# Kernel tuning notes

Hardware: AMD Instinct MI355X
Metric: run time of the kernel (lower is better)

## Reference

```python
import jax, jax.numpy as jnp
import numpy as np

LN_EPS = 1e-5


def _ln(h, g, b):
    mu = h.mean(-1, keepdims=True)
    var = ((h - mu) ** 2).mean(-1, keepdims=True)
    return (h - mu) / jnp.sqrt(var + LN_EPS) * g + b


def setup_inputs() -> dict:
    key = jax.random.key(0)
    ks = jax.random.split(key, 12)
    B, T, Cin, C, D, M = 16, 1024, 512, 1024, 256, 1024
    s = 0.02
    inp = {
        "x": jax.random.normal(ks[0], (B, T, Cin), jnp.float32),
        "masks": jnp.ones((B, T), jnp.float32),
        "W1": jax.random.normal(ks[1], (Cin, C), jnp.float32) * s,
        "g1": jnp.ones((C,), jnp.float32), "b1": jnp.zeros((C,), jnp.float32),
        "W2": jax.random.normal(ks[2], (C, C), jnp.float32) * s,
        "g2": jnp.ones((C,), jnp.float32), "b2": jnp.zeros((C,), jnp.float32),
        "W3": jax.random.normal(ks[3], (C, C), jnp.float32) * s,
        "g3": jnp.ones((C,), jnp.float32), "b3": jnp.zeros((C,), jnp.float32),
        "W4": jax.random.normal(ks[4], (C, C), jnp.float32) * s,
        "g4": jnp.ones((C,), jnp.float32), "b4": jnp.zeros((C,), jnp.float32),
        "W5": jax.random.normal(ks[5], (C, D), jnp.float32) * s,
        "b5": jnp.zeros((D,), jnp.float32),
        # Dirichlet(alpha=100) rows, as in the torch init: rows live on the simplex
        "embedding": jax.random.dirichlet(ks[6], jnp.full((D,), 100.0, jnp.float32), (M,)).astype(jnp.float32),
    }
    return inp


def reference(x, masks, W1, g1, b1, W2, g2, b2, W3, g3, b3, W4, g4, b4, W5, b5, embedding):
    h = jax.nn.relu(_ln(x @ W1, g1, b1))
    h = jax.nn.relu(_ln(h @ W2, g2, b2))
    h = jax.nn.relu(_ln(h @ W3, g3, b3))
    h = jax.nn.relu(_ln(h @ W4, g4, b4))
    z = h @ W5 + b5                              # [B, T, D]
    p = jax.nn.log_softmax(z, axis=-1)           # log-prob features

    B, T, D = p.shape
    p_flat = jax.lax.stop_gradient(p.reshape(-1, D))   # x.detach() in torch
    ep = jnp.exp(p_flat)                               # [N, D]
    # KL(exp(p) || e_m) summed over D, for all codes m:
    #   sum_d exp(p)*(p - log(e_m)) = rowsum(exp(p)*p) - exp(p) @ log(E)^T
    div = (ep * p_flat).sum(-1, keepdims=True) - ep @ jnp.log(embedding).T  # [N, M]
    idx = jnp.argmin(div, axis=-1)                     # [N]
    quant = jax.lax.stop_gradient(embedding[idx].reshape(B, T, D))

    # commitment loss: masked KL(exp(p) || quant.detach())
    kl = (jnp.exp(p) * (p - jnp.log(quant))).sum(-1)   # [B, T]
    loss = 0.25 * (kl * masks).mean(0).sum()

    # straight-through estimator
    q = p + jax.lax.stop_gradient(quant - p)
    return z, q, loss
```

## Files before the change

### kernel.cpp

```cpp
#include <hip/hip_runtime.h>
#include <hip/hip_bf16.h>
#include <stdint.h>

typedef __attribute__((ext_vector_type(4))) float f32x4;
typedef __attribute__((ext_vector_type(8))) __bf16 bf16x8;
typedef __attribute__((ext_vector_type(4))) __bf16 bf16x4;

#define LN_EPS 1e-5f

__device__ __forceinline__ void gload_lds16(const void* g, void* l) {
  __builtin_amdgcn_global_load_lds(
      (__attribute__((address_space(1))) void*)(uintptr_t)g,
      (__attribute__((address_space(3))) void*)(uint32_t)(uintptr_t)l,
      16, 0, 0);
}

__device__ __forceinline__ f32x4 mfma16(bf16x8 a, bf16x8 b, f32x4 c) {
  return __builtin_amdgcn_mfma_f32_16x16x32_bf16(a, b, c, 0, 0, 0);
}

__global__ __launch_bounds__(256) void k_cvt_bf16(const float* __restrict__ x,
                                                  __bf16* __restrict__ o) {
  int i = (blockIdx.x * 256 + threadIdx.x) * 8;
  f32x4 a = *(const f32x4*)(x + i);
  f32x4 b = *(const f32x4*)(x + i + 4);
  bf16x8 v;
#pragma unroll
  for (int j = 0; j < 4; ++j) { v[j] = (__bf16)a[j]; v[j + 4] = (__bf16)b[j]; }
  *(bf16x8*)(o + i) = v;
}

__global__ void k_transpose(const float* __restrict__ W, __bf16* __restrict__ Wt,
                            int K, int N) {
  __shared__ float t[32][33];
  int nt = blockIdx.x * 32, kt = blockIdx.y * 32;
  int tx = threadIdx.x, ty = threadIdx.y;
  t[ty][tx] = W[(size_t)(kt + ty) * N + nt + tx];
  __syncthreads();
  Wt[(size_t)(nt + ty) * K + kt + tx] = (__bf16)t[tx][ty];
}

__global__ void k_transpose3(const float* __restrict__ Wa, const float* __restrict__ Wb,
                             const float* __restrict__ Wc, __bf16* __restrict__ Ta,
                             __bf16* __restrict__ Tb, __bf16* __restrict__ Tc) {
  __shared__ float t[32][33];
  const float* W = blockIdx.z == 0 ? Wa : (blockIdx.z == 1 ? Wb : Wc);
  __bf16* T = blockIdx.z == 0 ? Ta : (blockIdx.z == 1 ? Tb : Tc);
  int nt = blockIdx.x * 32, kt = blockIdx.y * 32;
  int tx = threadIdx.x, ty = threadIdx.y;
  t[ty][tx] = W[(size_t)(kt + ty) * 1024 + nt + tx];
  __syncthreads();
  T[(size_t)(nt + ty) * 1024 + kt + tx] = (__bf16)t[tx][ty];
}

__global__ __launch_bounds__(256) void k_logE(const float* __restrict__ e,
                                              __bf16* __restrict__ o) {
  int i = blockIdx.x * 256 + threadIdx.x;
  o[i] = (__bf16)logf(e[i] * 256.0f);
}

__global__ __launch_bounds__(512, 2) void k_gemm256(
    const __bf16* __restrict__ A, const __bf16* __restrict__ Bt,
    __bf16* __restrict__ O, int N, int K) {
  __shared__ char lds[131072];
  const int tid = threadIdx.x;
  const int lane = tid & 63;
  const int wid = tid >> 6;
  const int wm = wid >> 2;
  const int wn = wid & 3;
  const int bm0 = blockIdx.x * 256;
  const int bn0 = blockIdx.y * 256;
  const int NT = K >> 6;

  const int slin = tid * 16;
  const int lrow = slin >> 7;
  const int scol = (slin & 127) ^ ((lrow & 7) << 4);
  const char* Ab = (const char*)A;
  const char* Bb = (const char*)Bt;
  const uint32_t rs = (uint32_t)K * 2;

  const int klo = (lane >> 4) * 16;
  const int sw = (lane & 7) << 4;
  const uint32_t kx0 = (uint32_t)(klo ^ sw);
  const uint32_t kx1 = (uint32_t)((64 + klo) ^ sw);
  const uint32_t abase = (uint32_t)(wm * 128 + (lane & 15)) * 128;
  const uint32_t bbase = (uint32_t)(wn * 64 + (lane & 15)) * 128;

  f32x4 acc[8][4];
#pragma unroll
  for (int i = 0; i < 8; ++i)
#pragma unroll
    for (int j = 0; j < 4; ++j) acc[i][j] = 0.0f;

#define LDSA(buf) (lds + (buf)*32768)
#define LDSB(buf) (lds + 65536 + (buf)*32768)
#define STAGE_A(t, h)                                                              \
  {                                                                                \
    const char* src = Ab + (size_t)(bm0 + (h)*128 + lrow) * rs + ((t) << 7) + scol;\
    char* dst = LDSA((t)&1) + (h)*16384 + slin;                                    \
    gload_lds16(src, dst);                                                         \
    gload_lds16(src + (size_t)64 * rs, dst + 8192);                                \
  }
#define STAGE_B(t, h)                                                              \
  {                                                                                \
    const char* src = Bb + (size_t)(bn0 + (h)*128 + lrow) * rs + ((t) << 7) + scol;\
    char* dst = LDSB((t)&1) + (h)*16384 + slin;                                    \
    gload_lds16(src, dst);                                                         \
    gload_lds16(src + (size_t)64 * rs, dst + 8192);                                \
  }

  STAGE_A(0, 0); STAGE_A(0, 1); STAGE_B(0, 0); STAGE_B(0, 1);
  STAGE_B(1, 0); STAGE_B(1, 1);
  asm volatile("s_waitcnt vmcnt(4)" ::: "memory");
  __builtin_amdgcn_s_barrier();
  asm volatile("" ::: "memory");

  for (int t = 0; t < NT; ++t) {
    const char* Acur = LDSA(t & 1);
    const char* Bcur = LDSB(t & 1);
    bf16x8 bF[4][2];
#pragma unroll
    for (int p = 0; p < 4; ++p) {
      const uint32_t ar = abase + (uint32_t)(2 * p) * 2048;
      bf16x8 a00 = *(const bf16x8*)(Acur + ar + kx0);
      bf16x8 a01 = *(const bf16x8*)(Acur + ar + kx1);
      bf16x8 a10 = *(const bf16x8*)(Acur + ar + 2048 + kx0);
      bf16x8 a11 = *(const bf16x8*)(Acur + ar + 2048 + kx1);
      if (p == 0) {
#pragma unroll
        for (int ni = 0; ni < 4; ++ni) {
          bF[ni][0] = *(const bf16x8*)(Bcur + bbase + ni * 2048 + kx0);
          bF[ni][1] = *(const bf16x8*)(Bcur + bbase + ni * 2048 + kx1);
        }
      }
      if (p == 0 && t + 1 < NT) STAGE_A(t + 1, 0);
      if (p == 1) {
        if (t + 1 < NT) STAGE_A(t + 1, 1);
        if (t + 2 < NT) STAGE_B(t + 2, 0);
      }
      if (p == 2 && t + 2 < NT) STAGE_B(t + 2, 1);

      asm volatile("" ::: "memory");
      __builtin_amdgcn_s_barrier();
      asm volatile("" ::: "memory");
      __builtin_amdgcn_s_setprio(1);
#pragma unroll
      for (int ni = 0; ni < 4; ++ni) {
        acc[2 * p][ni] = mfma16(a00, bF[ni][0], acc[2 * p][ni]);
        acc[2 * p][ni] = mfma16(a01, bF[ni][1], acc[2 * p][ni]);
        acc[2 * p + 1][ni] = mfma16(a10, bF[ni][0], acc[2 * p + 1][ni]);
        acc[2 * p + 1][ni] = mfma16(a11, bF[ni][1], acc[2 * p + 1][ni]);
      }
      __builtin_amdgcn_s_setprio(0);
      if (p == 3) asm volatile("s_waitcnt vmcnt(4)" ::: "memory");
      asm volatile("" ::: "memory");
      __builtin_amdgcn_s_barrier();
      asm volatile("" ::: "memory");
    }
  }
#undef STAGE_A
#undef STAGE_B
#undef LDSA
#undef LDSB

  const int r0 = (lane >> 4) * 4;
  const int cc = lane & 15;
#pragma unroll
  for (int mi = 0; mi < 8; ++mi) {
#pragma unroll
    for (int ni = 0; ni < 4; ++ni) {
      int r = bm0 + wm * 128 + mi * 16 + r0;
      int c = bn0 + wn * 64 + ni * 16 + cc;
#pragma unroll
      for (int j = 0; j < 4; ++j)
        O[(size_t)(r + j) * N + c] = (__bf16)acc[mi][ni][j];
    }
  }
}

template <int EPI>
__global__ __launch_bounds__(256) void k_gemm(
    const __bf16* __restrict__ A, const __bf16* __restrict__ Bt,
    void* __restrict__ outp, const float* __restrict__ bias,
    float* __restrict__ part_val, int* __restrict__ part_idx,
    int N, int K) {
  __shared__ char lds[32768];
  char* ldsA = lds;
  char* ldsB = lds + 16384;
  const int tid = threadIdx.x;
  const int lane = tid & 63;
  const int wid = tid >> 6;
  const int wm = wid >> 1, wn = wid & 1;
  const int bm0 = blockIdx.x * 128;
  const int bn0 = blockIdx.y * 128;

  const int slin = tid * 16;
  const int srow = slin >> 7;
  const int scol = (slin & 127) ^ ((srow & 7) << 4);

  const char* Ab = (const char*)A;
  const char* Bb = (const char*)Bt;
  const uint32_t rs = (uint32_t)K * 2;

  uint32_t ra[2][4], rb[2][4];
  {
    const int sw = (lane & 7) << 4;
    const int gk = lane & 48;
#pragma unroll
    for (int kk = 0; kk < 2; ++kk) {
#pragma unroll
      for (int i = 0; i < 4; ++i) {
        uint32_t kb = (uint32_t)((kk * 64 + gk) ^ sw);
        ra[kk][i] = (uint32_t)(wm * 64 + i * 16 + (lane & 15)) * 128 + kb;
        rb[kk][i] = (uint32_t)(wn * 64 + i * 16 + (lane & 15)) * 128 + kb;
      }
    }
  }

  f32x4 acc[4][4];
#pragma unroll
  for (int i = 0; i < 4; ++i)
#pragma unroll
    for (int j = 0; j < 4; ++j) acc[i][j] = 0.0f;

  for (int k0 = 0; k0 < K; k0 += 64) {
    __syncthreads();
    const uint32_t kbyte = (uint32_t)k0 * 2 + (uint32_t)scol;
#pragma unroll
    for (int i = 0; i < 4; ++i) {
      int row = i * 32 + srow;
      gload_lds16(Ab + (size_t)(bm0 + row) * rs + kbyte, ldsA + i * 4096 + slin);
    }
#pragma unroll
    for (int i = 0; i < 4; ++i) {
      int row = i * 32 + srow;
      gload_lds16(Bb + (size_t)(bn0 + row) * rs + kbyte, ldsB + i * 4096 + slin);
    }
    __syncthreads();
#pragma unroll
    for (int kk = 0; kk < 2; ++kk) {
      bf16x8 af[4], bfv[4];
#pragma unroll
      for (int i = 0; i < 4; ++i) af[i] = *(const bf16x8*)(ldsA + ra[kk][i]);
#pragma unroll
      for (int i = 0; i < 4; ++i) bfv[i] = *(const bf16x8*)(ldsB + rb[kk][i]);
#pragma unroll
      for (int mi = 0; mi < 4; ++mi)
#pragma unroll
        for (int ni = 0; ni < 4; ++ni)
          acc[mi][ni] = mfma16(af[mi], bfv[ni], acc[mi][ni]);
    }
  }

  const int r0 = (lane >> 4) * 4;
  const int cc = lane & 15;

  if constexpr (EPI == 1) {
    float* O = (float*)outp;
#pragma unroll
    for (int mi = 0; mi < 4; ++mi) {
#pragma unroll
      for (int ni = 0; ni < 4; ++ni) {
        int r = bm0 + wm * 64 + mi * 16 + r0;
        int c = bn0 + wn * 64 + ni * 16 + cc;
        float bv = bias[c];
#pragma unroll
        for (int j = 0; j < 4; ++j)
          O[(size_t)(r + j) * N + c] = acc[mi][ni][j] + bv;
      }
    }
  } else {
    const int nch = N >> 6;
#pragma unroll
    for (int mi = 0; mi < 4; ++mi) {
#pragma unroll
      for (int j = 0; j < 4; ++j) {
        float v = acc[mi][0][j];
        int c = cc;
#pragma unroll
        for (int ni = 1; ni < 4; ++ni) {
          float v2 = acc[mi][ni][j];
          int c2 = ni * 16 + cc;
          if (v2 > v) { v = v2; c = c2; }
        }
#pragma unroll
        for (int d = 1; d < 16; d <<= 1) {
          float ov = __shfl_xor(v, d);
          int oc = __shfl_xor(c, d);
          if (ov > v || (ov == v && oc < c)) { v = ov; c = oc; }
        }
        if (cc == 0) {
          int r = bm0 + wm * 64 + mi * 16 + r0 + j;
          int chunk = (bn0 >> 6) + wn;
          part_val[r * nch + chunk] = v;
          part_idx[r * nch + chunk] = bn0 + wn * 64 + c;
        }
      }
    }
  }
}

__global__ __launch_bounds__(256) void k_ln_relu(__bf16* __restrict__ h,
                                                 const float* __restrict__ g,
                                                 const float* __restrict__ b) {
  int lane = threadIdx.x & 63;
  int row = blockIdx.x * 4 + (threadIdx.x >> 6);
  __bf16* rp = h + (size_t)row * 1024;
  bf16x8 v0 = *(const bf16x8*)(rp + lane * 8);
  bf16x8 v1 = *(const bf16x8*)(rp + 512 + lane * 8);
  float f0[8], f1[8];
  float s = 0.f, sq = 0.f;
#pragma unroll
  for (int j = 0; j < 8; ++j) {
    f0[j] = (float)v0[j]; f1[j] = (float)v1[j];
    s += f0[j] + f1[j];
    sq += f0[j] * f0[j] + f1[j] * f1[j];
  }
#pragma unroll
  for (int d = 1; d < 64; d <<= 1) { s += __shfl_xor(s, d); sq += __shfl_xor(sq, d); }
  float mu = s * (1.0f / 1024.0f);
  float var = sq * (1.0f / 1024.0f) - mu * mu;
  float rstd = rsqrtf(var + LN_EPS);
  const f32x4* gv = (const f32x4*)g;
  const f32x4* bv = (const f32x4*)b;
  f32x4 ga0 = gv[lane * 2], ga1 = gv[lane * 2 + 1];
  f32x4 gb0 = gv[128 + lane * 2], gb1 = gv[128 + lane * 2 + 1];
  f32x4 ba0 = bv[lane * 2], ba1 = bv[lane * 2 + 1];
  f32x4 bb0 = bv[128 + lane * 2], bb1 = bv[128 + lane * 2 + 1];
  bf16x8 o0, o1;
#pragma unroll
  for (int j = 0; j < 4; ++j) {
    float t0 = (f0[j] - mu) * rstd * ga0[j] + ba0[j];
    float t1 = (f0[j + 4] - mu) * rstd * ga1[j] + ba1[j];
    float t2 = (f1[j] - mu) * rstd * gb0[j] + bb0[j];
    float t3 = (f1[j + 4] - mu) * rstd * gb1[j] + bb1[j];
    o0[j] = (__bf16)fmaxf(t0, 0.f);
    o0[j + 4] = (__bf16)fmaxf(t1, 0.f);
    o1[j] = (__bf16)fmaxf(t2, 0.f);
    o1[j + 4] = (__bf16)fmaxf(t3, 0.f);
  }
  *(bf16x8*)(rp + lane * 8) = o0;
  *(bf16x8*)(rp + 512 + lane * 8) = o1;
}

__global__ __launch_bounds__(256) void k_softmax(const float* __restrict__ z,
                                                 float* __restrict__ p,
                                                 __bf16* __restrict__ ep) {
  int lane = threadIdx.x & 63;
  int row = blockIdx.x * 4 + (threadIdx.x >> 6);
  f32x4 v = ((const f32x4*)(z + (size_t)row * 256))[lane];
  float m = fmaxf(fmaxf(v[0], v[1]), fmaxf(v[2], v[3]));
#pragma unroll
  for (int d = 1; d < 64; d <<= 1) m = fmaxf(m, __shfl_xor(m, d));
  f32x4 e;
  float s = 0.f;
#pragma unroll
  for (int j = 0; j < 4; ++j) { e[j] = expf(v[j] - m); s += e[j]; }
#pragma unroll
  for (int d = 1; d < 64; d <<= 1) s += __shfl_xor(s, d);
  float ls = logf(s);
  float inv = 1.0f / s;
  f32x4 pv;
  bf16x4 ev;
#pragma unroll
  for (int j = 0; j < 4; ++j) { pv[j] = v[j] - m - ls; ev[j] = (__bf16)(e[j] * inv); }
  ((f32x4*)(p + (size_t)row * 256))[lane] = pv;
  ((bf16x4*)(ep + (size_t)row * 256))[lane] = ev;
}

__global__ __launch_bounds__(256) void k_final(
    const float* __restrict__ part_val, const int* __restrict__ part_idx,
    const float* __restrict__ p, const float* __restrict__ emb,
    const float* __restrict__ masks, float* __restrict__ q,
    float* __restrict__ blockloss) {
  __shared__ float ls[4];
  int lane = threadIdx.x & 63;
  int w = threadIdx.x >> 6;
  int row = blockIdx.x * 4 + w;
  float v = -3.4e38f;
  int c = 0x7fffffff;
  if (lane < 16) { v = part_val[row * 16 + lane]; c = part_idx[row * 16 + lane]; }
#pragma unroll
  for (int d = 1; d < 16; d <<= 1) {
    float ov = __shfl_xor(v, d);
    int oc = __shfl_xor(c, d);
    if (ov > v || (ov == v && oc < c)) { v = ov; c = oc; }
  }
  int code = __shfl(c, 0);
  f32x4 ev = ((const f32x4*)(emb + (size_t)code * 256))[lane];
  ((f32x4*)(q + (size_t)row * 256))[lane] = ev;
  f32x4 pv = ((const f32x4*)(p + (size_t)row * 256))[lane];
  float kl = 0.f;
#pragma unroll
  for (int j = 0; j < 4; ++j) kl += expf(pv[j]) * (pv[j] - logf(ev[j]));
#pragma unroll
  for (int d = 1; d < 64; d <<= 1) kl += __shfl_xor(kl, d);
  if (lane == 0) ls[w] = kl * masks[row];
  __syncthreads();
  if (threadIdx.x == 0) blockloss[blockIdx.x] = ls[0] + ls[1] + ls[2] + ls[3];
}

__global__ __launch_bounds__(256) void k_loss_reduce(const float* __restrict__ bl,
                                                     float* __restrict__ out) {
  __shared__ float s[256];
  float a = 0.f;
#pragma unroll
  for (int i = 0; i < 16; ++i) a += bl[threadIdx.x + i * 256];
  s[threadIdx.x] = a;
  __syncthreads();
  for (int st = 128; st > 0; st >>= 1) {
    if (threadIdx.x < st) s[threadIdx.x] += s[threadIdx.x + st];
    __syncthreads();
  }
  if (threadIdx.x == 0) out[0] = s[0] * (0.25f / 16.0f);
}

extern "C" void kernel_launch(void* const* d_in, const int* in_sizes, int n_in,
                              void* d_out, int out_size, void* d_ws, size_t ws_size,
                              hipStream_t stream) {
  const float* x = (const float*)d_in[0];
  const float* masks = (const float*)d_in[1];
  const float* W1 = (const float*)d_in[2];
  const float* g1 = (const float*)d_in[3];
  const float* b1 = (const float*)d_in[4];
  const float* W2 = (const float*)d_in[5];
  const float* g2 = (const float*)d_in[6];
  const float* b2 = (const float*)d_in[7];
  const float* W3 = (const float*)d_in[8];
  const float* g3 = (const float*)d_in[9];
  const float* b3 = (const float*)d_in[10];
  const float* W4 = (const float*)d_in[11];
  const float* g4 = (const float*)d_in[12];
  const float* b4 = (const float*)d_in[13];
  const float* W5 = (const float*)d_in[14];
  const float* b5 = (const float*)d_in[15];
  const float* emb = (const float*)d_in[16];

  const int M = 16384;
  char* ws = (char*)d_ws;
  __bf16* bufA = (__bf16*)(ws);
  __bf16* bufB = (__bf16*)(ws + (32ull << 20));
  __bf16* W1t = (__bf16*)(ws + (64ull << 20));
  __bf16* W2t = (__bf16*)(ws + (65ull << 20));
  __bf16* W3t = (__bf16*)(ws + (67ull << 20));
  __bf16* W4t = (__bf16*)(ws + (69ull << 20));
  __bf16* W5t = (__bf16*)(ws + (71ull << 20));
  __bf16* logE = (__bf16*)(ws + (72ull << 20));
  float* part_val = (float*)(ws + (73ull << 20));
  int* part_idx = (int*)(ws + (74ull << 20));
  float* blockloss = (float*)(ws + (75ull << 20));
  float* p = (float*)(ws);
  __bf16* ep = (__bf16*)(ws + (16ull << 20));

  float* z = (float*)d_out;
  float* q = z + (size_t)M * 256;
  float* lossp = z + 2ull * M * 256;

  dim3 tb32(32, 32);
  k_cvt_bf16<<<4096, 256, 0, stream>>>(x, bufB);
  k_transpose<<<dim3(32, 16), tb32, 0, stream>>>(W1, W1t, 512, 1024);
  k_transpose3<<<dim3(32, 32, 3), tb32, 0, stream>>>(W2, W3, W4, W2t, W3t, W4t);
  k_transpose<<<dim3(8, 32), tb32, 0, stream>>>(W5, W5t, 1024, 256);
  k_logE<<<1024, 256, 0, stream>>>(emb, logE);

  k_gemm256<<<dim3(64, 4), 512, 0, stream>>>(bufB, W1t, bufA, 1024, 512);
  k_ln_relu<<<4096, 256, 0, stream>>>(bufA, g1, b1);
  k_gemm256<<<dim3(64, 4), 512, 0, stream>>>(bufA, W2t, bufB, 1024, 1024);
  k_ln_relu<<<4096, 256, 0, stream>>>(bufB, g2, b2);
  k_gemm256<<<dim3(64, 4), 512, 0, stream>>>(bufB, W3t, bufA, 1024, 1024);
  k_ln_relu<<<4096, 256, 0, stream>>>(bufA, g3, b3);
  k_gemm256<<<dim3(64, 4), 512, 0, stream>>>(bufA, W4t, bufB, 1024, 1024);
  k_ln_relu<<<4096, 256, 0, stream>>>(bufB, g4, b4);
  k_gemm<1><<<dim3(128, 2), 256, 0, stream>>>(bufB, W5t, z, b5, nullptr, nullptr, 256, 1024);
  k_softmax<<<4096, 256, 0, stream>>>(z, p, ep);
  k_gemm<2><<<dim3(128, 8), 256, 0, stream>>>(ep, logE, nullptr, nullptr, part_val, part_idx, 1024, 256);
  k_final<<<4096, 256, 0, stream>>>(part_val, part_idx, p, emb, masks, q, blockloss);
  k_loss_reduce<<<1, 256, 0, stream>>>(blockloss, lossp);
}
```

Before: 273.4 us.

## Fuse final projection GEMM with log-softmax and swizzle GEMM block order

The final Linear(C,D) GEMM now computes the full 256-wide output row per block and runs log-softmax in its epilogue. It writes z, bf16 probabilities and a per-row log-sum-exp, so the separate softmax kernel and the float p buffer are gone, and k_final rebuilds p from z minus the log-sum-exp. The 256x256 GEMMs also use a 1D grid with a swizzled block-to-tile mapping so that concurrently running blocks share A/B tiles in cache. The fused kernel uses 64-row tiles and loads all of W5 per k-step, which could lower MFMA efficiency for that GEMM.

Measured after the change: 281.4 us. 2.9% more time.

```diff
diff --git a/kernel.cpp b/kernel.cpp
--- a/kernel.cpp
+++ b/kernel.cpp
@@ -68,8 +68,9 @@
   const int wid = tid >> 6;
   const int wm = wid >> 2;
   const int wn = wid & 3;
-  const int bm0 = blockIdx.x * 256;
-  const int bn0 = blockIdx.y * 256;
+  const int swz = ((blockIdx.x & 7) << 5) | (blockIdx.x >> 3);
+  const int bm0 = (swz & 63) * 256;
+  const int bn0 = (swz >> 6) * 256;
   const int NT = K >> 6;
 
   const int slin = tid * 16;
@@ -174,128 +175,6 @@
 #pragma unroll
       for (int j = 0; j < 4; ++j)
         O[(size_t)(r + j) * N + c] = (__bf16)acc[mi][ni][j];
-    }
-  }
-}
-
-template <int EPI>
-__global__ __launch_bounds__(256) void k_gemm(
-    const __bf16* __restrict__ A, const __bf16* __restrict__ Bt,
-    void* __restrict__ outp, const float* __restrict__ bias,
-    float* __restrict__ part_val, int* __restrict__ part_idx,
-    int N, int K) {
-  __shared__ char lds[32768];
-  char* ldsA = lds;
-  char* ldsB = lds + 16384;
-  const int tid = threadIdx.x;
-  const int lane = tid & 63;
-  const int wid = tid >> 6;
-  const int wm = wid >> 1, wn = wid & 1;
-  const int bm0 = blockIdx.x * 128;
-  const int bn0 = blockIdx.y * 128;
-
-  const int slin = tid * 16;
-  const int srow = slin >> 7;
-  const int scol = (slin & 127) ^ ((srow & 7) << 4);
-
-  const char* Ab = (const char*)A;
-  const char* Bb = (const char*)Bt;
-  const uint32_t rs = (uint32_t)K * 2;
-
-  uint32_t ra[2][4], rb[2][4];
-  {
-    const int sw = (lane & 7) << 4;
-    const int gk = lane & 48;
-#pragma unroll
-    for (int kk = 0; kk < 2; ++kk) {
-#pragma unroll
-      for (int i = 0; i < 4; ++i) {
-        uint32_t kb = (uint32_t)((kk * 64 + gk) ^ sw);
-        ra[kk][i] = (uint32_t)(wm * 64 + i * 16 + (lane & 15)) * 128 + kb;
-        rb[kk][i] = (uint32_t)(wn * 64 + i * 16 + (lane & 15)) * 128 + kb;
-      }
-    }
-  }
-
-  f32x4 acc[4][4];
-#pragma unroll
-  for (int i = 0; i < 4; ++i)
-#pragma unroll
-    for (int j = 0; j < 4; ++j) acc[i][j] = 0.0f;
-
-  for (int k0 = 0; k0 < K; k0 += 64) {
-    __syncthreads();
-    const uint32_t kbyte = (uint32_t)k0 * 2 + (uint32_t)scol;
-#pragma unroll
-    for (int i = 0; i < 4; ++i) {
-      int row = i * 32 + srow;
-      gload_lds16(Ab + (size_t)(bm0 + row) * rs + kbyte, ldsA + i * 4096 + slin);
-    }
-#pragma unroll
-    for (int i = 0; i < 4; ++i) {
-      int row = i * 32 + srow;
-      gload_lds16(Bb + (size_t)(bn0 + row) * rs + kbyte, ldsB + i * 4096 + slin);
-    }
-    __syncthreads();
-#pragma unroll
-    for (int kk = 0; kk < 2; ++kk) {
-      bf16x8 af[4], bfv[4];
-#pragma unroll
-      for (int i = 0; i < 4; ++i) af[i] = *(const bf16x8*)(ldsA + ra[kk][i]);
-#pragma unroll
-      for (int i = 0; i < 4; ++i) bfv[i] = *(const bf16x8*)(ldsB + rb[kk][i]);
-#pragma unroll
-      for (int mi = 0; mi < 4; ++mi)
-#pragma unroll
-        for (int ni = 0; ni < 4; ++ni)
-          acc[mi][ni] = mfma16(af[mi], bfv[ni], acc[mi][ni]);
-    }
-  }
-
-  const int r0 = (lane >> 4) * 4;
-  const int cc = lane & 15;
-
-  if constexpr (EPI == 1) {
-    float* O = (float*)outp;
-#pragma unroll
-    for (int mi = 0; mi < 4; ++mi) {
-#pragma unroll
-      for (int ni = 0; ni < 4; ++ni) {
-        int r = bm0 + wm * 64 + mi * 16 + r0;
-        int c = bn0 + wn * 64 + ni * 16 + cc;
-        float bv = bias[c];
-#pragma unroll
-        for (int j = 0; j < 4; ++j)
-          O[(size_t)(r + j) * N + c] = acc[mi][ni][j] + bv;
-      }
-    }
-  } else {
-    const int nch = N >> 6;
-#pragma unroll
-    for (int mi = 0; mi < 4; ++mi) {
-#pragma unroll
-      for (int j = 0; j < 4; ++j) {
-        float v = acc[mi][0][j];
-        int c = cc;
-#pragma unroll
-        for (int ni = 1; ni < 4; ++ni) {
-          float v2 = acc[mi][ni][j];
-          int c2 = ni * 16 + cc;
-          if (v2 > v) { v = v2; c = c2; }
-        }
-#pragma unroll
-        for (int d = 1; d < 16; d <<= 1) {
-          float ov = __shfl_xor(v, d);
-          int oc = __shfl_xor(c, d);
-          if (ov > v || (ov == v && oc < c)) { v = ov; c = oc; }
-        }
-        if (cc == 0) {
-          int r = bm0 + wm * 64 + mi * 16 + r0 + j;
-          int chunk = (bn0 >> 6) + wn;
-          part_val[r * nch + chunk] = v;
-          part_idx[r * nch + chunk] = bn0 + wn * 64 + c;
-        }
-      }
     }
   }
 }
@@ -343,36 +222,257 @@
   *(bf16x8*)(rp + 512 + lane * 8) = o1;
 }
 
-__global__ __launch_bounds__(256) void k_softmax(const float* __restrict__ z,
-                                                 float* __restrict__ p,
-                                                 __bf16* __restrict__ ep) {
-  int lane = threadIdx.x & 63;
-  int row = blockIdx.x * 4 + (threadIdx.x >> 6);
-  f32x4 v = ((const f32x4*)(z + (size_t)row * 256))[lane];
-  float m = fmaxf(fmaxf(v[0], v[1]), fmaxf(v[2], v[3]));
-#pragma unroll
-  for (int d = 1; d < 64; d <<= 1) m = fmaxf(m, __shfl_xor(m, d));
-  f32x4 e;
-  float s = 0.f;
-#pragma unroll
-  for (int j = 0; j < 4; ++j) { e[j] = expf(v[j] - m); s += e[j]; }
-#pragma unroll
-  for (int d = 1; d < 64; d <<= 1) s += __shfl_xor(s, d);
-  float ls = logf(s);
-  float inv = 1.0f / s;
-  f32x4 pv;
-  bf16x4 ev;
-#pragma unroll
-  for (int j = 0; j < 4; ++j) { pv[j] = v[j] - m - ls; ev[j] = (__bf16)(e[j] * inv); }
-  ((f32x4*)(p + (size_t)row * 256))[lane] = pv;
-  ((bf16x4*)(ep + (size_t)row * 256))[lane] = ev;
+__global__ __launch_bounds__(256) void k_gemm_sm(
+    const __bf16* __restrict__ A, const __bf16* __restrict__ Bt,
+    const float* __restrict__ bias, float* __restrict__ z,
+    __bf16* __restrict__ ep, float* __restrict__ sm) {
+  const int K = 1024;
+  __shared__ char lds[40960];
+  char* ldsA = lds;
+  char* ldsB = lds + 8192;
+  const int tid = threadIdx.x;
+  const int lane = tid & 63;
+  const int wn = tid >> 6;
+  const int bm0 = blockIdx.x * 64;
+  const char* Ab = (const char*)A;
+  const char* Bb = (const char*)Bt;
+  const uint32_t rs = (uint32_t)K * 2;
+
+  const int cc = lane & 15;
+  uint32_t ra[2][4], rb[2][4];
+  {
+    const int sww = (lane & 7) << 4;
+    const int gk = lane & 48;
+#pragma unroll
+    for (int kk = 0; kk < 2; ++kk) {
+#pragma unroll
+      for (int i = 0; i < 4; ++i) {
+        uint32_t kb = (uint32_t)((kk * 64 + gk) ^ sww);
+        ra[kk][i] = (uint32_t)(i * 16 + cc) * 128 + kb;
+        rb[kk][i] = (uint32_t)(wn * 64 + i * 16 + cc) * 128 + kb;
+      }
+    }
+  }
+
+  f32x4 acc[4][4];
+#pragma unroll
+  for (int i = 0; i < 4; ++i)
+#pragma unroll
+    for (int j = 0; j < 4; ++j) acc[i][j] = 0.0f;
+
+  for (int k0 = 0; k0 < K; k0 += 64) {
+    __syncthreads();
+#pragma unroll
+    for (int i = 0; i < 2; ++i) {
+      int lin = i * 4096 + tid * 16;
+      int row = lin >> 7;
+      int col = (lin & 127) ^ ((row & 7) << 4);
+      gload_lds16(Ab + (size_t)(bm0 + row) * rs + k0 * 2 + col, ldsA + lin);
+    }
+#pragma unroll
+    for (int i = 0; i < 8; ++i) {
+      int lin = i * 4096 + tid * 16;
+      int row = lin >> 7;
+      int col = (lin & 127) ^ ((row & 7) << 4);
+      gload_lds16(Bb + (size_t)row * rs + k0 * 2 + col, ldsB + lin);
+    }
+    __syncthreads();
+#pragma unroll
+    for (int kk = 0; kk < 2; ++kk) {
+      bf16x8 af[4], bfv[4];
+#pragma unroll
+      for (int i = 0; i < 4; ++i) af[i] = *(const bf16x8*)(ldsA + ra[kk][i]);
+#pragma unroll
+      for (int i = 0; i < 4; ++i) bfv[i] = *(const bf16x8*)(ldsB + rb[kk][i]);
+#pragma unroll
+      for (int mi = 0; mi < 4; ++mi)
+#pragma unroll
+        for (int ni = 0; ni < 4; ++ni)
+          acc[mi][ni] = mfma16(af[mi], bfv[ni], acc[mi][ni]);
+    }
+  }
+
+  __syncthreads();
+  float* stm = (float*)lds;
+  float* sts = (float*)(lds + 1024);
+  float* rowm = (float*)(lds + 2048);
+  float* rows_ = (float*)(lds + 2304);
+
+  const int r0 = (lane >> 4) * 4;
+  float bvv[4];
+#pragma unroll
+  for (int ni = 0; ni < 4; ++ni) bvv[ni] = bias[wn * 64 + ni * 16 + cc];
+
+  float zv[4][4];
+#pragma unroll
+  for (int mi = 0; mi < 4; ++mi) {
+#pragma unroll
+    for (int j = 0; j < 4; ++j) {
+      float m = -3.4e38f;
+#pragma unroll
+      for (int ni = 0; ni < 4; ++ni) {
+        zv[mi][ni] = acc[mi][ni][j] + bvv[ni];
+        m = fmaxf(m, zv[mi][ni]);
+      }
+#pragma unroll
+      for (int d = 1; d < 16; d <<= 1) m = fmaxf(m, __shfl_xor(m, d));
+      if (cc == 0) stm[wn * 64 + mi * 16 + r0 + j] = m;
+    }
+  }
+  __syncthreads();
+  if (tid < 64) {
+    float m = fmaxf(fmaxf(stm[tid], stm[64 + tid]), fmaxf(stm[128 + tid], stm[192 + tid]));
+    rowm[tid] = m;
+  }
+  __syncthreads();
+#pragma unroll
+  for (int mi = 0; mi < 4; ++mi) {
+#pragma unroll
+    for (int j = 0; j < 4; ++j) {
+      int r = mi * 16 + r0 + j;
+      float m = rowm[r];
+      float s = 0.f;
+#pragma unroll
+      for (int ni = 0; ni < 4; ++ni) s += expf(acc[mi][ni][j] + bvv[ni] - m);
+#pragma unroll
+      for (int d = 1; d < 16; d <<= 1) s += __shfl_xor(s, d);
+      if (cc == 0) sts[wn * 64 + r] = s;
+    }
+  }
+  __syncthreads();
+  if (tid < 64) {
+    float s = sts[tid] + sts[64 + tid] + sts[128 + tid] + sts[192 + tid];
+    rows_[tid] = s;
+    sm[bm0 + tid] = rowm[tid] + logf(s);
+  }
+  __syncthreads();
+#pragma unroll
+  for (int mi = 0; mi < 4; ++mi) {
+#pragma unroll
+    for (int j = 0; j < 4; ++j) {
+      int r = mi * 16 + r0 + j;
+      float m = rowm[r];
+      float inv = 1.0f / rows_[r];
+      float* zp = z + (size_t)(bm0 + r) * 256;
+      __bf16* epp = ep + (size_t)(bm0 + r) * 256;
+#pragma unroll
+      for (int ni = 0; ni < 4; ++ni) {
+        int c = wn * 64 + ni * 16 + cc;
+        float zz = acc[mi][ni][j] + bvv[ni];
+        zp[c] = zz;
+        epp[c] = (__bf16)(expf(zz - m) * inv);
+      }
+    }
+  }
+}
+
+__global__ __launch_bounds__(256) void k_gemm_div(
+    const __bf16* __restrict__ A, const __bf16* __restrict__ Bt,
+    float* __restrict__ part_val, int* __restrict__ part_idx, int N, int K) {
+  __shared__ char lds[32768];
+  char* ldsA = lds;
+  char* ldsB = lds + 16384;
+  const int tid = threadIdx.x;
+  const int lane = tid & 63;
+  const int wid = tid >> 6;
+  const int wm = wid >> 1, wn = wid & 1;
+  const int bm0 = blockIdx.x * 128;
+  const int bn0 = blockIdx.y * 128;
+
+  const int slin = tid * 16;
+  const int srow = slin >> 7;
+  const int scol = (slin & 127) ^ ((srow & 7) << 4);
+
+  const char* Ab = (const char*)A;
+  const char* Bb = (const char*)Bt;
+  const uint32_t rs = (uint32_t)K * 2;
+
+  uint32_t ra[2][4], rb[2][4];
+  {
+    const int sw = (lane & 7) << 4;
+    const int gk = lane & 48;
+#pragma unroll
+    for (int kk = 0; kk < 2; ++kk) {
+#pragma unroll
+      for (int i = 0; i < 4; ++i) {
+        uint32_t kb = (uint32_t)((kk * 64 + gk) ^ sw);
+        ra[kk][i] = (uint32_t)(wm * 64 + i * 16 + (lane & 15)) * 128 + kb;
+        rb[kk][i] = (uint32_t)(wn * 64 + i * 16 + (lane & 15)) * 128 + kb;
+      }
+    }
+  }
+
+  f32x4 acc[4][4];
+#pragma unroll
+  for (int i = 0; i < 4; ++i)
+#pragma unroll
+    for (int j = 0; j < 4; ++j) acc[i][j] = 0.0f;
+
+  for (int k0 = 0; k0 < K; k0 += 64) {
+    __syncthreads();
+    const uint32_t kbyte = (uint32_t)k0 * 2 + (uint32_t)scol;
+#pragma unroll
+    for (int i = 0; i < 4; ++i) {
+      int row = i * 32 + srow;
+      gload_lds16(Ab + (size_t)(bm0 + row) * rs + kbyte, ldsA + i * 4096 + slin);
+    }
+#pragma unroll
+    for (int i = 0; i < 4; ++i) {
+      int row = i * 32 + srow;
+      gload_lds16(Bb + (size_t)(bn0 + row) * rs + kbyte, ldsB + i * 4096 + slin);
+    }
+    __syncthreads();
+#pragma unroll
+    for (int kk = 0; kk < 2; ++kk) {
+      bf16x8 af[4], bfv[4];
+#pragma unroll
+      for (int i = 0; i < 4; ++i) af[i] = *(const bf16x8*)(ldsA + ra[kk][i]);
+#pragma unroll
+      for (int i = 0; i < 4; ++i) bfv[i] = *(const bf16x8*)(ldsB + rb[kk][i]);
+#pragma unroll
+      for (int mi = 0; mi < 4; ++mi)
+#pragma unroll
+        for (int ni = 0; ni < 4; ++ni)
+          acc[mi][ni] = mfma16(af[mi], bfv[ni], acc[mi][ni]);
+    }
+  }
+
+  const int r0 = (lane >> 4) * 4;
+  const int cc = lane & 15;
+  const int nch = N >> 6;
+#pragma unroll
+  for (int mi = 0; mi < 4; ++mi) {
+#pragma unroll
+    for (int j = 0; j < 4; ++j) {
+      float v = acc[mi][0][j];
+      int c = cc;
+#pragma unroll
+      for (int ni = 1; ni < 4; ++ni) {
+        float v2 = acc[mi][ni][j];
+        int c2 = ni * 16 + cc;
+        if (v2 > v) { v = v2; c = c2; }
+      }
+#pragma unroll
+      for (int d = 1; d < 16; d <<= 1) {
+        float ov = __shfl_xor(v, d);
+        int oc = __shfl_xor(c, d);
+        if (ov > v || (ov == v && oc < c)) { v = ov; c = oc; }
+      }
+      if (cc == 0) {
+        int r = bm0 + wm * 64 + mi * 16 + r0 + j;
+        int chunk = (bn0 >> 6) + wn;
+        part_val[r * nch + chunk] = v;
+        part_idx[r * nch + chunk] = bn0 + wn * 64 + c;
+      }
+    }
+  }
 }
 
 __global__ __launch_bounds__(256) void k_final(
     const float* __restrict__ part_val, const int* __restrict__ part_idx,
-    const float* __restrict__ p, const float* __restrict__ emb,
-    const float* __restrict__ masks, float* __restrict__ q,
-    float* __restrict__ blockloss) {
+    const float* __restrict__ z, const float* __restrict__ sm,
+    const float* __restrict__ emb, const float* __restrict__ masks,
+    float* __restrict__ q, float* __restrict__ blockloss) {
   __shared__ float ls[4];
   int lane = threadIdx.x & 63;
   int w = threadIdx.x >> 6;
@@ -389,10 +489,14 @@
   int code = __shfl(c, 0);
   f32x4 ev = ((const f32x4*)(emb + (size_t)code * 256))[lane];
   ((f32x4*)(q + (size_t)row * 256))[lane] = ev;
-  f32x4 pv = ((const f32x4*)(p + (size_t)row * 256))[lane];
+  f32x4 zv = ((const f32x4*)(z + (size_t)row * 256))[lane];
+  float smr = sm[row];
   float kl = 0.f;
 #pragma unroll
-  for (int j = 0; j < 4; ++j) kl += expf(pv[j]) * (pv[j] - logf(ev[j]));
+  for (int j = 0; j < 4; ++j) {
+    float pj = zv[j] - smr;
+    kl += expf(pj) * (pj - logf(ev[j]));
+  }
 #pragma unroll
   for (int d = 1; d < 64; d <<= 1) kl += __shfl_xor(kl, d);
   if (lane == 0) ls[w] = kl * masks[row];
@@ -449,7 +553,7 @@
   float* part_val = (float*)(ws + (73ull << 20));
   int* part_idx = (int*)(ws + (74ull << 20));
   float* blockloss = (float*)(ws + (75ull << 20));
-  float* p = (float*)(ws);
+  float* sm = (float*)(ws + (76ull << 20));
   __bf16* ep = (__bf16*)(ws + (16ull << 20));
 
   float* z = (float*)d_out;
@@ -463,17 +567,16 @@
   k_transpose<<<dim3(8, 32), tb32, 0, stream>>>(W5, W5t, 1024, 256);
   k_logE<<<1024, 256, 0, stream>>>(emb, logE);
 
-  k_gemm256<<<dim3(64, 4), 512, 0, stream>>>(bufB, W1t, bufA, 1024, 512);
+  k_gemm256<<<256, 512, 0, stream>>>(bufB, W1t, bufA, 1024, 512);
   k_ln_relu<<<4096, 256, 0, stream>>>(bufA, g1, b1);
-  k_gemm256<<<dim3(64, 4), 512, 0, stream>>>(bufA, W2t, bufB, 1024, 1024);
+  k_gemm256<<<256, 512, 0, stream>>>(bufA, W2t, bufB, 1024, 1024);
   k_ln_relu<<<4096, 256, 0, stream>>>(bufB, g2, b2);
-  k_gemm256<<<dim3(64, 4), 512, 0, stream>>>(bufB, W3t, bufA, 1024, 1024);
+  k_gemm256<<<256, 512, 0, stream>>>(bufB, W3t, bufA, 1024, 1024);
   k_ln_relu<<<4096, 256, 0, stream>>>(bufA, g3, b3);
-  k_gemm256<<<dim3(64, 4), 512, 0, stream>>>(bufA, W4t, bufB, 1024, 1024);
+  k_gemm256<<<256, 512, 0, stream>>>(bufA, W4t, bufB, 1024, 1024);
   k_ln_relu<<<4096, 256, 0, stream>>>(bufB, g4, b4);
-  k_gemm<1><<<dim3(128, 2), 256, 0, stream>>>(bufB, W5t, z, b5, nullptr, nullptr, 256, 1024);
-  k_softmax<<<4096, 256, 0, stream>>>(z, p, ep);
-  k_gemm<2><<<dim3(128, 8), 256, 0, stream>>>(ep, logE, nullptr, nullptr, part_val, part_idx, 1024, 256);
-  k_final<<<4096, 256, 0, stream>>>(part_val, part_idx, p, emb, masks, q, blockloss);
+  k_gemm_sm<<<256, 256, 0, stream>>>(bufB, W5t, b5, z, ep, sm);
+  k_gemm_div<<<dim3(128, 8), 256, 0, stream>>>(ep, logE, part_val, part_idx, 1024, 256);
+  k_final<<<4096, 256, 0, stream>>>(part_val, part_idx, z, sm, emb, masks, q, blockloss);
   k_loss_reduce<<<1, 256, 0, stream>>>(blockloss, lossp);
 }
```
